# Optimization experiments

Measured on AMD Instinct MI355X. Metric: run time of the kernel, lower is better.

Reference implementation:

```python
import jax, jax.numpy as jnp
import numpy as np

N = 30000   # nodes
E = 240000  # edges
G = 16      # graphs in batch
DIMS = [1, 256, 512, 1024]
OUT = 1024

def _xavier(key, fan_in, fan_out):
    lim = float(np.sqrt(6.0 / (fan_in + fan_out)))
    return jax.random.uniform(key, (fan_in, fan_out), minval=-lim, maxval=lim, dtype=jnp.float32)

def setup_inputs() -> dict:
    key = jax.random.key(0)
    ks = jax.random.split(key, 8)
    x = jax.random.normal(ks[0], (N, DIMS[0]), dtype=jnp.float32)
    edge_index = jax.random.randint(ks[1], (2, E), 0, N, dtype=jnp.int64)
    batch = jnp.sort(jax.random.randint(ks[2], (N,), 0, G, dtype=jnp.int64))
    W1 = _xavier(ks[3], DIMS[0], DIMS[1]); b1 = jnp.zeros((DIMS[1],), jnp.float32)
    W2 = _xavier(ks[4], DIMS[1], DIMS[2]); b2 = jnp.zeros((DIMS[2],), jnp.float32)
    W3 = _xavier(ks[5], DIMS[2], DIMS[3]); b3 = jnp.zeros((DIMS[3],), jnp.float32)
    Wo = _xavier(ks[6], DIMS[3], OUT);     bo = jnp.zeros((OUT,), jnp.float32)
    return {"x": x, "edge_index": edge_index, "batch": batch,
            "W1": W1, "b1": b1, "W2": W2, "b2": b2, "W3": W3, "b3": b3,
            "Wo": Wo, "bo": bo}

def reference(x, edge_index, batch, W1, b1, W2, b2, W3, b3, Wo, bo):
    n = x.shape[0]
    loops = jnp.arange(n)
    # GCNConv adds self-loops, then symmetric deg^-1/2 normalization
    src = jnp.concatenate([edge_index[0], loops])
    dst = jnp.concatenate([edge_index[1], loops])
    deg = jnp.zeros((n,), jnp.float32).at[dst].add(1.0)  # >=1 due to self-loops
    dis = jax.lax.rsqrt(deg)
    norm = (dis[src] * dis[dst])[:, None]  # [E+N, 1]

    def gcn(h, W, b):
        h = h @ W                                   # linear (no bias in lin)
        agg = jnp.zeros_like(h).at[dst].add(h[src] * norm)  # scatter-add messages
        return agg + b                              # GCNConv bias

    h = jax.nn.relu(gcn(x, W1, b1))
    h = jax.nn.relu(gcn(h, W2, b2))
    h = jax.nn.relu(gcn(h, W3, b3))
    # global mean pool over graphs
    sums = jnp.zeros((G, h.shape[1]), h.dtype).at[batch].add(h)
    cnt = jnp.zeros((G,), h.dtype).at[batch].add(1.0)
    pooled = sums / jnp.maximum(cnt, 1.0)[:, None]
    return pooled @ Wo + bo
```

## Files before the change

kernel.cpp:

```cpp
#include <hip/hip_runtime.h>
#include <hip/hip_bf16.h>
#include <stdint.h>

#define N_NODES 30000
#define E_EDGES 240000
#define NGRAPH  16
#define D1      256
#define D2      512
#define D3      1024
#define DOUT    1024
#define M_PAD   30720
#define NT_M    240
#define CAP     40

typedef unsigned short ushort_t;
typedef short short8 __attribute__((ext_vector_type(8)));
typedef float f32x4 __attribute__((ext_vector_type(4)));

__device__ __forceinline__ float bf2f(ushort_t u) {
    union { unsigned int i; float f; } v; v.i = ((unsigned int)u) << 16; return v.f;
}
__device__ __forceinline__ ushort_t f2bf(float x) {
    union { float f; unsigned int i; } v; v.f = x;
    unsigned int r = v.i + 0x7fffu + ((v.i >> 16) & 1u);
    return (ushort_t)(r >> 16);
}

__device__ __forceinline__ void gl_lds16(const ushort_t* g, ushort_t* l) {
    __builtin_amdgcn_global_load_lds(
        (const __attribute__((address_space(1))) void*)(g),
        (__attribute__((address_space(3))) void*)(l), 16, 0, 0);
}

__global__ void k_detect(const void* w1, const void* ei, int* flags) {
    int lane = threadIdx.x & 63;
    const ushort_t* h = (const ushort_t*)w1;
    float v = fabsf(bf2f(h[lane * 2]));
    unsigned long long badf = __ballot(!(v <= 0.25f));
    const int* e = (const int*)ei;
    unsigned long long badi = __ballot(e[lane * 2 + 1] != 0);
    if (threadIdx.x == 0) {
        flags[0] = (badf == 0ull) ? 1 : 0;
        flags[1] = (badi == 0ull) ? 1 : 0;
    }
}

__global__ void k_setup(const void* x, const void* batch, const void* w1, const void* b1,
                        const void* b2, const void* b3, const void* bo,
                        const void* W2, const void* W3,
                        float* xf, int* batch32, float* W1f, float* b1f, float* b2f,
                        float* b3f, float* bof, ushort_t* Wt2, ushort_t* Wt3,
                        int* slotcnt, float* pooled, float* pooled2, const int* flags) {
    int isbf = flags[0];
    int bid = blockIdx.x;
    int tid = threadIdx.x;
    if (bid < 492) {
        int i = bid * 256 + tid;
        if (i < 3072) {
            const void* src; float* dst; int idx;
            if      (i < 256)  { src = w1; dst = W1f; idx = i; }
            else if (i < 512)  { src = b1; dst = b1f; idx = i - 256; }
            else if (i < 1024) { src = b2; dst = b2f; idx = i - 512; }
            else if (i < 2048) { src = b3; dst = b3f; idx = i - 1024; }
            else               { src = bo; dst = bof; idx = i - 2048; }
            dst[idx] = isbf ? bf2f(((const ushort_t*)src)[idx]) : ((const float*)src)[idx];
        } else if (i < 33072) {
            int idx = i - 3072;
            xf[idx] = isbf ? bf2f(((const ushort_t*)x)[idx]) : ((const float*)x)[idx];
        } else if (i < 63072) {
            int idx = i - 33072;
            batch32[idx] = flags[1] ? (int)((const long long*)batch)[idx]
                                    : ((const int*)batch)[idx];
        } else if (i < 93072) {
            slotcnt[i - 63072] = 0;
        } else if (i < 109456) {
            pooled[i - 93072] = 0.0f;
        } else if (i < 125840) {
            pooled2[i - 109456] = 0.0f;
        }
    } else {
        __shared__ ushort_t tile[32][33];
        int tb = bid - 492;
        const void* in; ushort_t* out; int R, C, bx, by;
        if (tb < 128) { in = W2; out = Wt2; R = D1; C = D2; bx = tb & 15; by = tb >> 4; }
        else { tb -= 128; in = W3; out = Wt3; R = D2; C = D3; bx = tb & 31; by = tb >> 5; }
        int tx = tid & 31, ty = tid >> 5;
        int c0 = bx * 32, r0 = by * 32;
        for (int i = ty; i < 32; i += 8) {
            size_t idx = (size_t)(r0 + i) * C + c0 + tx;
            tile[i][tx] = isbf ? ((const ushort_t*)in)[idx] : f2bf(((const float*)in)[idx]);
        }
        __syncthreads();
        for (int i = ty; i < 32; i += 8) out[(size_t)(c0 + i) * R + r0 + tx] = tile[tx][i];
    }
}

__global__ void k_edge_count(const void* ei, int* slotcnt, int* slots, const int* flags) {
    int e = blockIdx.x * 256 + threadIdx.x;
    if (e >= E_EDGES) return;
    int s, d;
    if (flags[1]) {
        s = (int)((const long long*)ei)[e];
        d = (int)((const long long*)ei)[E_EDGES + e];
    } else {
        s = ((const int*)ei)[e];
        d = ((const int*)ei)[E_EDGES + e];
    }
    if ((unsigned)s >= N_NODES || (unsigned)d >= N_NODES) return;
    int pos = atomicAdd(&slotcnt[d], 1);
    if (pos < CAP) slots[d * CAP + pos] = s;
}

__global__ void k_s1(const float* xf, const int* slotcnt, const int* slots,
                     const int* batch, float* dis, float* s1, float* cntg) {
    int b = blockIdx.x;
    if (b == 118) {
        int g = threadIdx.x;
        if (g >= NGRAPH) return;
        int lo0 = 0, hi0 = N_NODES;
        while (lo0 < hi0) { int m = (lo0 + hi0) >> 1; if (batch[m] < g) lo0 = m + 1; else hi0 = m; }
        int lo1 = lo0, hi1 = N_NODES;
        while (lo1 < hi1) { int m = (lo1 + hi1) >> 1; if (batch[m] < g + 1) lo1 = m + 1; else hi1 = m; }
        cntg[g] = (float)(lo1 - lo0);
        return;
    }
    int d = b * 256 + threadIdx.x;
    if (d >= N_NODES) return;
    int cd = slotcnt[d];
    float di = rsqrtf(1.0f + (float)cd);
    dis[d] = di;
    int cnt = cd < CAP ? cd : CAP;
    float acc = xf[d] * di;
    for (int k = 0; k < cnt; k++) {
        int s = slots[d * CAP + k];
        acc += xf[s] * rsqrtf(1.0f + (float)slotcnt[s]);
    }
    s1[d] = acc * di;
}

__global__ void k_agg1(const float* s1, const float* W1f, const float* b1f,
                       ushort_t* a2, const int* slots, const int* slotcnt, const float* dis) {
    int node = blockIdx.x * 4 + (threadIdx.x >> 6);
    int lane = threadIdx.x & 63;
    int c4 = lane * 4;
    float w[4], bb[4], a[4];
    #pragma unroll
    for (int j = 0; j < 4; j++) { w[j] = W1f[c4 + j]; bb[j] = b1f[c4 + j]; }
    float di = dis[node];
    int cnt = slotcnt[node]; cnt = cnt < CAP ? cnt : CAP;
    float sv = s1[node];
    float wsl = di * di;
    #pragma unroll
    for (int j = 0; j < 4; j++) a[j] = wsl * fmaxf(sv * w[j] + bb[j], 0.0f);
    for (int k = 0; k < cnt; k++) {
        int s = slots[node * CAP + k];
        float ss = s1[s];
        float wn = dis[s] * di;
        #pragma unroll
        for (int j = 0; j < 4; j++) a[j] += wn * fmaxf(ss * w[j] + bb[j], 0.0f);
    }
    uint2 o;
    o.x = (unsigned int)f2bf(a[0]) | ((unsigned int)f2bf(a[1]) << 16);
    o.y = (unsigned int)f2bf(a[2]) | ((unsigned int)f2bf(a[3]) << 16);
    *(uint2*)&a2[(size_t)node * D1 + c4] = o;
}

__global__ void k_agg2(const ushort_t* h, ushort_t* out, const int* slots,
                       const int* slotcnt, const float* dis) {
    int node = blockIdx.x * 4 + (threadIdx.x >> 6);
    int lane = threadIdx.x & 63;
    int c8 = lane * 8;
    float di = dis[node];
    int cnt = slotcnt[node]; cnt = cnt < CAP ? cnt : CAP;
    float w = di * di;
    const ushort_t* hp = h + c8;
    short8 p = *(const short8*)&hp[(size_t)node * D2];
    float a[8];
    #pragma unroll
    for (int j = 0; j < 8; j++) a[j] = w * bf2f((ushort_t)p[j]);
    if (cnt > 0) {
        int s0 = slots[node * CAP];
        short8 q0 = *(const short8*)&hp[(size_t)s0 * D2];
        float ws0 = dis[s0] * di;
        for (int k = 1; k < cnt; k++) {
            int s1i = slots[node * CAP + k];
            short8 q1 = *(const short8*)&hp[(size_t)s1i * D2];
            float ws1 = dis[s1i] * di;
            #pragma unroll
            for (int j = 0; j < 8; j++) a[j] += ws0 * bf2f((ushort_t)q0[j]);
            q0 = q1; ws0 = ws1;
        }
        #pragma unroll
        for (int j = 0; j < 8; j++) a[j] += ws0 * bf2f((ushort_t)q0[j]);
    }
    uint4 o;
    o.x = (unsigned int)f2bf(a[0]) | ((unsigned int)f2bf(a[1]) << 16);
    o.y = (unsigned int)f2bf(a[2]) | ((unsigned int)f2bf(a[3]) << 16);
    o.z = (unsigned int)f2bf(a[4]) | ((unsigned int)f2bf(a[5]) << 16);
    o.w = (unsigned int)f2bf(a[6]) | ((unsigned int)f2bf(a[7]) << 16);
    *(uint4*)&out[(size_t)node * D2 + c8] = o;
}

__global__ __launch_bounds__(256, 3) void k_gemm(const ushort_t* A, const ushort_t* Bt,
                                                 const float* bias, ushort_t* Cmat,
                                                 int K, int Ncols, int ntn) {
    __shared__ __align__(16) ushort_t As[2][128 * 32];
    __shared__ __align__(16) ushort_t Bs[2][128 * 32];
    int tid = threadIdx.x;
    int id = blockIdx.x;
    int xcd = id & 7, q = id >> 3;
    int rt = xcd * (NT_M / 8) + q / ntn;
    int ct = q % ntn;
    int bm0 = rt * 128, bn0 = ct * 128;
    int wave = tid >> 6, lane = tid & 63;
    int wm = (wave & 1) * 64, wn = (wave >> 1) * 64;
    int l15 = lane & 15, quad = lane >> 4;

    int m1 = tid >> 2, k1 = (tid & 3) << 3;
    int m2 = m1 + 64;
    int off1 = m1 * 32 + k1, off2 = m2 * 32 + k1;
    const ushort_t* pA1 = A + (size_t)(bm0 + m1) * K + k1;
    const ushort_t* pA2 = A + (size_t)(bm0 + m2) * K + k1;
    const ushort_t* pB1 = Bt + (size_t)(bn0 + m1) * K + k1;
    const ushort_t* pB2 = Bt + (size_t)(bn0 + m2) * K + k1;

    {
        uint4 la0 = *(const uint4*)pA1, la1 = *(const uint4*)pA2;
        uint4 lb0 = *(const uint4*)pB1, lb1 = *(const uint4*)pB2;
        *(uint4*)&As[0][off1] = la0; *(uint4*)&As[0][off2] = la1;
        *(uint4*)&Bs[0][off1] = lb0; *(uint4*)&Bs[0][off2] = lb1;
    }

    f32x4 acc[4][4];
    for (int a = 0; a < 4; a++)
        for (int b = 0; b < 4; b++)
            acc[a][b] = (f32x4){0.f, 0.f, 0.f, 0.f};

    int niter = K >> 5;
    for (int it = 0; it < niter; ++it) {
        __syncthreads();
        int ktn = (it + 1) << 5;
        uint4 na0, na1, nb0, nb1;
        if (ktn < K) {
            na0 = *(const uint4*)(pA1 + ktn); na1 = *(const uint4*)(pA2 + ktn);
            nb0 = *(const uint4*)(pB1 + ktn); nb1 = *(const uint4*)(pB2 + ktn);
        }
        int cb = it & 1;
        short8 af[4], bfr[4];
        for (int im = 0; im < 4; im++)
            af[im] = *(const short8*)&As[cb][(wm + im * 16 + l15) * 32 + quad * 8];
        for (int in = 0; in < 4; in++)
            bfr[in] = *(const short8*)&Bs[cb][(wn + in * 16 + l15) * 32 + quad * 8];
        for (int im = 0; im < 4; im++)
            for (int in = 0; in < 4; in++)
                acc[im][in] = __builtin_amdgcn_mfma_f32_16x16x32_bf16(af[im], bfr[in], acc[im][in], 0, 0, 0);
        if (ktn < K) {
            int wb = cb ^ 1;
            *(uint4*)&As[wb][off1] = na0; *(uint4*)&As[wb][off2] = na1;
            *(uint4*)&Bs[wb][off1] = nb0; *(uint4*)&Bs[wb][off2] = nb1;
        }
    }

    for (int im = 0; im < 4; im++) {
        int row = bm0 + wm + im * 16 + quad * 4;
        for (int in = 0; in < 4; in++) {
            int col = bn0 + wn + in * 16 + l15;
            float bv = bias[col];
            for (int r = 0; r < 4; r++) {
                float v = acc[im][in][r] + bv;
                v = v > 0.0f ? v : 0.0f;
                Cmat[(size_t)(row + r) * Ncols + col] = f2bf(v);
            }
        }
    }
}

#define GPHASE(M0, M1, PRESTAGE, TAILWAIT)                                             \
    a0 = rdA(slot, M0, inrow0); a1 = rdA(slot, M0, inrow1);                            \
    a2r = rdA(slot, M1, inrow0); a3r = rdA(slot, M1, inrow1);                          \
    PRESTAGE                                                                           \
    asm volatile("" ::: "memory");                                                     \
    __builtin_amdgcn_s_barrier();                                                      \
    asm volatile("s_waitcnt lgkmcnt(0)" ::: "memory");                                 \
    __builtin_amdgcn_sched_barrier(0);                                                 \
    __builtin_amdgcn_s_setprio(1);                                                     \
    _Pragma("unroll")                                                                  \
    for (int n = 0; n < 4; ++n) {                                                      \
        acc[M0][n] = __builtin_amdgcn_mfma_f32_16x16x32_bf16(a0,  bf_[n][0], acc[M0][n], 0, 0, 0); \
        acc[M0][n] = __builtin_amdgcn_mfma_f32_16x16x32_bf16(a1,  bf_[n][1], acc[M0][n], 0, 0, 0); \
        acc[M1][n] = __builtin_amdgcn_mfma_f32_16x16x32_bf16(a2r, bf_[n][0], acc[M1][n], 0, 0, 0); \
        acc[M1][n] = __builtin_amdgcn_mfma_f32_16x16x32_bf16(a3r, bf_[n][1], acc[M1][n], 0, 0, 0); \
    }                                                                                  \
    __builtin_amdgcn_s_setprio(0);                                                     \
    TAILWAIT                                                                           \
    asm volatile("" ::: "memory");                                                     \
    __builtin_amdgcn_s_barrier();

#define PS_ALL  if (hn) { stage_unit(nslot, t + 1, 0); stage_unit(nslot, t + 1, 1);    \
                          stage_unit(nslot, t + 1, 2); stage_unit(nslot, t + 1, 3); }
#define PS_NONE
#define TW_NONE
#define TW_P2 if (hn) { asm volatile("s_waitcnt vmcnt(8)" ::: "memory"); } \
              else    { asm volatile("s_waitcnt vmcnt(0)" ::: "memory"); }
#define TW_P4 if (hn) { asm volatile("s_waitcnt vmcnt(2)" ::: "memory"); }

__global__ __launch_bounds__(512, 2) void k_gemm8p(const ushort_t* A, const ushort_t* Bt,
                                                   const float* bias, const int* batch,
                                                   float* pooled, int K, int ntn, int NT) {
    __shared__ __align__(16) ushort_t As[2][256 * 64];
    __shared__ __align__(16) ushort_t Bs[2][256 * 64];
    const int tid = threadIdx.x;
    const int id = blockIdx.x;
    const int xcd = id & 7, q = id >> 3;
    const int rt = xcd * ((M_PAD / 256) / 8) + q / ntn;
    const int ct = q % ntn;
    const int bm0 = rt * 256, bn0 = ct * 256;
    const int wave = tid >> 6, lane = tid & 63;
    const int wr = wave >> 2, wc = wave & 3;
    const int l15 = lane & 15, quad = lane >> 4;

    const ushort_t* gA = A + (size_t)bm0 * K;
    const ushort_t* gB = Bt + (size_t)bn0 * K;

    auto stage_blk = [&](ushort_t* ldsbase, const ushort_t* gbase, int kt, int b) {
        int row = b >> 3;
        int kb = (b & 7) ^ (row & 7);
        gl_lds16(gbase + (size_t)row * K + (kt << 6) + (kb << 3), ldsbase + (b << 3));
    };
    auto stage_unit = [&](int slot, int kt, int u) {
        if (u == 0)      { stage_blk(Bs[slot], gB, kt, tid);        stage_blk(Bs[slot], gB, kt, tid + 512); }
        else if (u == 1) { stage_blk(Bs[slot], gB, kt, tid + 1024); stage_blk(Bs[slot], gB, kt, tid + 1536); }
        else if (u == 2) { stage_blk(As[slot], gA, kt, tid);        stage_blk(As[slot], gA, kt, tid + 1024); }
        else             { stage_blk(As[slot], gA, kt, tid + 512);  stage_blk(As[slot], gA, kt, tid + 1536); }
    };

    const int swzx = (l15 & 7) << 4;
    const int inrow0 = (quad * 16) ^ swzx;
    const int inrow1 = (quad * 16 + 64) ^ swzx;
    const int arowb = (wr * 128 + l15) * 128;
    const int browb = (wc * 64 + l15) * 128;

    auto rdA = [&](int slot, int m, int inr) -> short8 {
        return *(const short8*)((const char*)As[slot] + arowb + m * 2048 + inr);
    };
    auto rdB = [&](int slot, int n, int inr) -> short8 {
        return *(const short8*)((const char*)Bs[slot] + browb + n * 2048 + inr);
    };

    stage_unit(0, 0, 0); stage_unit(0, 0, 1); stage_unit(0, 0, 2); stage_unit(0, 0, 3);
    asm volatile("s_waitcnt vmcnt(2)" ::: "memory");
    __builtin_amdgcn_s_barrier();

    f32x4 acc[8][4];
    #pragma unroll
    for (int a = 0; a < 8; a++)
        #pragma unroll
        for (int b = 0; b < 4; b++)
            acc[a][b] = (f32x4){0.f, 0.f, 0.f, 0.f};

    short8 bf_[4][2];
    for (int t = 0; t < NT; ++t) {
        const int slot = t & 1, nslot = slot ^ 1;
        const bool hn = (t + 1) < NT;
        short8 a0, a1, a2r, a3r;
        #pragma unroll
        for (int n = 0; n < 4; ++n) {
            bf_[n][0] = rdB(slot, n, inrow0);
            bf_[n][1] = rdB(slot, n, inrow1);
        }
        GPHASE(0, 1, PS_ALL, TW_NONE)
        GPHASE(2, 3, PS_NONE, TW_P2)
        GPHASE(4, 5, PS_NONE, TW_NONE)
        GPHASE(6, 7, PS_NONE, TW_P4)
    }

    asm volatile("s_waitcnt vmcnt(0) lgkmcnt(0)" ::: "memory");
    __syncthreads();
    float* pl = (float*)&As[0][0];
    int* gtile = (int*)&Bs[0][0];
    for (int i = tid; i < NGRAPH * 256; i += 512) pl[i] = 0.0f;
    if (tid < 256) {
        int r = bm0 + tid; if (r > N_NODES - 1) r = N_NODES - 1;
        int g = batch[r]; g = g < 0 ? 0 : (g > NGRAPH - 1 ? NGRAPH - 1 : g);
        gtile[tid] = g;
    }
    __syncthreads();

    int gmin = gtile[0], gmax = gtile[255];
    if (gmin == gmax && bm0 + 255 < N_NODES) {
        float csum[4];
        float bv[4];
        #pragma unroll
        for (int in = 0; in < 4; in++) {
            csum[in] = 0.0f;
            bv[in] = bias[bn0 + wc * 64 + in * 16 + l15];
        }
        #pragma unroll
        for (int im = 0; im < 8; im++) {
            #pragma unroll
            for (int in = 0; in < 4; in++) {
                #pragma unroll
                for (int r = 0; r < 4; r++)
                    csum[in] += fmaxf(acc[im][in][r] + bv[in], 0.0f);
            }
        }
        #pragma unroll
        for (int in = 0; in < 4; in++) {
            csum[in] += __shfl_xor(csum[in], 16);
            csum[in] += __shfl_xor(csum[in], 32);
        }
        if (quad == 0) {
            #pragma unroll
            for (int in = 0; in < 4; in++)
                atomicAdd(&pl[gmin * 256 + wc * 64 + in * 16 + l15], csum[in]);
        }
    } else {
        #pragma unroll
        for (int im = 0; im < 8; im++) {
            int rl = wr * 128 + im * 16 + quad * 4;
            #pragma unroll
            for (int in = 0; in < 4; in++) {
                int cl = wc * 64 + in * 16 + l15;
                float bv = bias[bn0 + cl];
                float vsum = 0.0f;
                int gprev = gtile[rl];
                #pragma unroll
                for (int r = 0; r < 4; r++) {
                    int row = bm0 + rl + r;
                    float v = (row < N_NODES) ? fmaxf(acc[im][in][r] + bv, 0.0f) : 0.0f;
                    int g = gtile[rl + r];
                    if (g != gprev) {
                        atomicAdd(&pl[gprev * 256 + cl], vsum);
                        vsum = 0.0f; gprev = g;
                    }
                    vsum += v;
                }
                atomicAdd(&pl[gprev * 256 + cl], vsum);
            }
        }
    }
    __syncthreads();

    int span = (gmax - gmin + 1) * 256;
    for (int idx = tid; idx < span; idx += 512) {
        int g = gmin + (idx >> 8), cl = idx & 255;
        float v = pl[g * 256 + cl];
        if (v != 0.0f) atomicAdd(&pooled[g * DOUT + bn0 + cl], v);
    }
}

__global__ __launch_bounds__(256) void k_out_partial(const float* pooled, const void* Wo,
                                                     float* pooled2, const int* flags) {
    __shared__ float pl[NGRAPH * 32];
    int tid = threadIdx.x;
    int col = blockIdx.x * 256 + tid;
    int k0 = blockIdx.y * 32;
    for (int i = tid; i < NGRAPH * 32; i += 256) {
        int g = i >> 5, kk = i & 31;
        pl[i] = pooled[g * D3 + k0 + kk];
    }
    __syncthreads();
    int isbf = flags[0];
    float acc[NGRAPH];
    #pragma unroll
    for (int g = 0; g < NGRAPH; g++) acc[g] = 0.0f;
    #pragma unroll 4
    for (int kk = 0; kk < 32; kk++) {
        int k = k0 + kk;
        float wv = isbf ? bf2f(((const ushort_t*)Wo)[(size_t)k * DOUT + col])
                        : ((const float*)Wo)[(size_t)k * DOUT + col];
        #pragma unroll
        for (int g = 0; g < NGRAPH; g++)
            acc[g] += pl[g * 32 + kk] * wv;
    }
    #pragma unroll
    for (int g = 0; g < NGRAPH; g++)
        atomicAdd(&pooled2[g * DOUT + col], acc[g]);
}

__global__ void k_out_fin(const float* pooled2, const float* bof, const float* cntg,
                          void* out, const int* flags) {
    int i = blockIdx.x * 256 + threadIdx.x;
    int g = i >> 10, o = i & 1023;
    float c = cntg[g]; c = c > 1.0f ? c : 1.0f;
    float v = pooled2[i] / c + bof[o];
    if (flags[0]) ((ushort_t*)out)[i] = f2bf(v);
    else          ((float*)out)[i] = v;
}

extern "C" void kernel_launch(void* const* d_in, const int* in_sizes, int n_in,
                              void* d_out, int out_size, void* d_ws, size_t ws_size,
                              hipStream_t stream) {
    const void* x_raw  = d_in[0];
    const void* ei_raw = d_in[1];
    const void* b_raw  = d_in[2];
    const void* W1_raw = d_in[3];
    const void* b1_raw = d_in[4];
    const void* W2_raw = d_in[5];
    const void* b2_raw = d_in[6];
    const void* W3_raw = d_in[7];
    const void* b3_raw = d_in[8];
    const void* Wo_raw = d_in[9];
    const void* bo_raw = d_in[10];

    char* w = (char*)d_ws;
    size_t off = 0;
    auto alloc = [&](size_t b) { size_t o = off; off += (b + 255) & ~(size_t)255; return o; };
    int*   flags   = (int*)  (w + alloc(256));
    float* xf      = (float*)(w + alloc((size_t)N_NODES * 4));
    int*   batch32 = (int*)  (w + alloc((size_t)N_NODES * 4));
    float* W1f     = (float*)(w + alloc(D1 * 4));
    float* b1f     = (float*)(w + alloc(D1 * 4));
    float* b2f     = (float*)(w + alloc(D2 * 4));
    float* b3f     = (float*)(w + alloc(D3 * 4));
    float* bof     = (float*)(w + alloc(DOUT * 4));
    float* dis     = (float*)(w + alloc((size_t)N_NODES * 4));
    float* s1      = (float*)(w + alloc((size_t)N_NODES * 4));
    float* cntg    = (float*)(w + alloc(64));
    float* pooled  = (float*)(w + alloc((size_t)NGRAPH * DOUT * 4));
    float* pooled2 = (float*)(w + alloc((size_t)NGRAPH * DOUT * 4));
    int*   slotcnt = (int*)  (w + alloc((size_t)N_NODES * 4));
    int*   slots   = (int*)  (w + alloc((size_t)N_NODES * CAP * 4));
    ushort_t* Wt2  = (ushort_t*)(w + alloc((size_t)D2 * D1 * 2));
    ushort_t* Wt3  = (ushort_t*)(w + alloc((size_t)D3 * D2 * 2));
    ushort_t* slabA = (ushort_t*)(w + alloc((size_t)M_PAD * D2 * 2));
    ushort_t* a2 = slabA;
    ushort_t* a3 = slabA;
    ushort_t* h2   = (ushort_t*)(w + alloc((size_t)M_PAD * D2 * 2));

    int nb_e = (E_EDGES + 255) / 256;

    k_detect<<<1, 64, 0, stream>>>(W1_raw, ei_raw, flags);
    k_setup<<<1132, 256, 0, stream>>>(x_raw, b_raw, W1_raw, b1_raw, b2_raw, b3_raw, bo_raw,
                                      W2_raw, W3_raw, xf, batch32, W1f, b1f, b2f, b3f, bof,
                                      Wt2, Wt3, slotcnt, pooled, pooled2, flags);
    k_edge_count<<<nb_e, 256, 0, stream>>>(ei_raw, slotcnt, slots, flags);
    k_s1<<<119, 256, 0, stream>>>(xf, slotcnt, slots, batch32, dis, s1, cntg);

    k_agg1<<<N_NODES / 4, 256, 0, stream>>>(s1, W1f, b1f, a2, slots, slotcnt, dis);
    k_gemm<<<NT_M * (D2 / 128), 256, 0, stream>>>(a2, Wt2, b2f, h2, D1, D2, D2 / 128);
    k_agg2<<<N_NODES / 4, 256, 0, stream>>>(h2, a3, slots, slotcnt, dis);
    k_gemm8p<<<(M_PAD / 256) * (D3 / 256), 512, 0, stream>>>(a3, Wt3, b3f, batch32,
                                                             pooled, D2, D3 / 256, D2 / 64);

    k_out_partial<<<dim3(DOUT / 256, D3 / 32), 256, 0, stream>>>(pooled, Wo_raw, pooled2, flags);
    k_out_fin<<<NGRAPH * DOUT / 256, 256, 0, stream>>>(pooled2, bof, cntg, d_out, flags);
}
```

Before: 272.3 us.

## Broadcast neighbor indices via shuffles and simplify fused GEMM pipeline

In the two aggregation kernels, each lane now loads one neighbor slot index and its normalization weight up front, and the neighbor loop pulls these with wave shuffles. This replaces the serial per-iteration loads of slot, dis and s1. Separately, the fused layer-3 GEMM+pool kernel drops its hand-scheduled phase macros (split staging, explicit vmcnt waits, setprio, sched barriers) in favor of a plain double-buffered loop: stage the next tile, run the MFMAs, then __syncthreads. This simplifies the code but risks losing the fine-grained overlap of global-to-LDS loads with MFMA work.

New measurement: 254.8 us. 1.07x faster.

```diff
diff --git a/kernel.cpp b/kernel.cpp
--- a/kernel.cpp
+++ b/kernel.cpp
@@ -148,14 +148,16 @@
     for (int j = 0; j < 4; j++) { w[j] = W1f[c4 + j]; bb[j] = b1f[c4 + j]; }
     float di = dis[node];
     int cnt = slotcnt[node]; cnt = cnt < CAP ? cnt : CAP;
+    int s_l = (lane < cnt) ? slots[node * CAP + lane] : 0;
+    float wn_l = dis[s_l] * di;
+    float ss_l = s1[s_l];
     float sv = s1[node];
     float wsl = di * di;
     #pragma unroll
     for (int j = 0; j < 4; j++) a[j] = wsl * fmaxf(sv * w[j] + bb[j], 0.0f);
     for (int k = 0; k < cnt; k++) {
-        int s = slots[node * CAP + k];
-        float ss = s1[s];
-        float wn = dis[s] * di;
+        float ss = __shfl(ss_l, k);
+        float wn = __shfl(wn_l, k);
         #pragma unroll
         for (int j = 0; j < 4; j++) a[j] += wn * fmaxf(ss * w[j] + bb[j], 0.0f);
     }
@@ -172,6 +174,8 @@
     int c8 = lane * 8;
     float di = dis[node];
     int cnt = slotcnt[node]; cnt = cnt < CAP ? cnt : CAP;
+    int s_l = (lane < cnt) ? slots[node * CAP + lane] : 0;
+    float ws_l = dis[s_l] * di;
     float w = di * di;
     const ushort_t* hp = h + c8;
     short8 p = *(const short8*)&hp[(size_t)node * D2];
@@ -179,13 +183,13 @@
     #pragma unroll
     for (int j = 0; j < 8; j++) a[j] = w * bf2f((ushort_t)p[j]);
     if (cnt > 0) {
-        int s0 = slots[node * CAP];
+        int s0 = __shfl(s_l, 0);
+        float ws0 = __shfl(ws_l, 0);
         short8 q0 = *(const short8*)&hp[(size_t)s0 * D2];
-        float ws0 = dis[s0] * di;
         for (int k = 1; k < cnt; k++) {
-            int s1i = slots[node * CAP + k];
-            short8 q1 = *(const short8*)&hp[(size_t)s1i * D2];
-            float ws1 = dis[s1i] * di;
+            int sk = __shfl(s_l, k);
+            float ws1 = __shfl(ws_l, k);
+            short8 q1 = *(const short8*)&hp[(size_t)sk * D2];
             #pragma unroll
             for (int j = 0; j < 8; j++) a[j] += ws0 * bf2f((ushort_t)q0[j]);
             q0 = q1; ws0 = ws1;
@@ -275,38 +279,9 @@
     }
 }
 
-#define GPHASE(M0, M1, PRESTAGE, TAILWAIT)                                             \
-    a0 = rdA(slot, M0, inrow0); a1 = rdA(slot, M0, inrow1);                            \
-    a2r = rdA(slot, M1, inrow0); a3r = rdA(slot, M1, inrow1);                          \
-    PRESTAGE                                                                           \
-    asm volatile("" ::: "memory");                                                     \
-    __builtin_amdgcn_s_barrier();                                                      \
-    asm volatile("s_waitcnt lgkmcnt(0)" ::: "memory");                                 \
-    __builtin_amdgcn_sched_barrier(0);                                                 \
-    __builtin_amdgcn_s_setprio(1);                                                     \
-    _Pragma("unroll")                                                                  \
-    for (int n = 0; n < 4; ++n) {                                                      \
-        acc[M0][n] = __builtin_amdgcn_mfma_f32_16x16x32_bf16(a0,  bf_[n][0], acc[M0][n], 0, 0, 0); \
-        acc[M0][n] = __builtin_amdgcn_mfma_f32_16x16x32_bf16(a1,  bf_[n][1], acc[M0][n], 0, 0, 0); \
-        acc[M1][n] = __builtin_amdgcn_mfma_f32_16x16x32_bf16(a2r, bf_[n][0], acc[M1][n], 0, 0, 0); \
-        acc[M1][n] = __builtin_amdgcn_mfma_f32_16x16x32_bf16(a3r, bf_[n][1], acc[M1][n], 0, 0, 0); \
-    }                                                                                  \
-    __builtin_amdgcn_s_setprio(0);                                                     \
-    TAILWAIT                                                                           \
-    asm volatile("" ::: "memory");                                                     \
-    __builtin_amdgcn_s_barrier();
-
-#define PS_ALL  if (hn) { stage_unit(nslot, t + 1, 0); stage_unit(nslot, t + 1, 1);    \
-                          stage_unit(nslot, t + 1, 2); stage_unit(nslot, t + 1, 3); }
-#define PS_NONE
-#define TW_NONE
-#define TW_P2 if (hn) { asm volatile("s_waitcnt vmcnt(8)" ::: "memory"); } \
-              else    { asm volatile("s_waitcnt vmcnt(0)" ::: "memory"); }
-#define TW_P4 if (hn) { asm volatile("s_waitcnt vmcnt(2)" ::: "memory"); }
-
-__global__ __launch_bounds__(512, 2) void k_gemm8p(const ushort_t* A, const ushort_t* Bt,
-                                                   const float* bias, const int* batch,
-                                                   float* pooled, int K, int ntn, int NT) {
+__global__ __launch_bounds__(512, 2) void k_gemm_pool(const ushort_t* A, const ushort_t* Bt,
+                                                      const float* bias, const int* batch,
+                                                      float* pooled, int K, int ntn, int NT) {
     __shared__ __align__(16) ushort_t As[2][256 * 64];
     __shared__ __align__(16) ushort_t Bs[2][256 * 64];
     const int tid = threadIdx.x;
@@ -327,11 +302,11 @@
         int kb = (b & 7) ^ (row & 7);
         gl_lds16(gbase + (size_t)row * K + (kt << 6) + (kb << 3), ldsbase + (b << 3));
     };
-    auto stage_unit = [&](int slot, int kt, int u) {
-        if (u == 0)      { stage_blk(Bs[slot], gB, kt, tid);        stage_blk(Bs[slot], gB, kt, tid + 512); }
-        else if (u == 1) { stage_blk(Bs[slot], gB, kt, tid + 1024); stage_blk(Bs[slot], gB, kt, tid + 1536); }
-        else if (u == 2) { stage_blk(As[slot], gA, kt, tid);        stage_blk(As[slot], gA, kt, tid + 1024); }
-        else             { stage_blk(As[slot], gA, kt, tid + 512);  stage_blk(As[slot], gA, kt, tid + 1536); }
+    auto stage_all = [&](int slot, int kt) {
+        stage_blk(Bs[slot], gB, kt, tid);        stage_blk(Bs[slot], gB, kt, tid + 512);
+        stage_blk(Bs[slot], gB, kt, tid + 1024); stage_blk(Bs[slot], gB, kt, tid + 1536);
+        stage_blk(As[slot], gA, kt, tid);        stage_blk(As[slot], gA, kt, tid + 512);
+        stage_blk(As[slot], gA, kt, tid + 1024); stage_blk(As[slot], gA, kt, tid + 1536);
     };
 
     const int swzx = (l15 & 7) << 4;
@@ -347,9 +322,8 @@
         return *(const short8*)((const char*)Bs[slot] + browb + n * 2048 + inr);
     };
 
-    stage_unit(0, 0, 0); stage_unit(0, 0, 1); stage_unit(0, 0, 2); stage_unit(0, 0, 3);
-    asm volatile("s_waitcnt vmcnt(2)" ::: "memory");
-    __builtin_amdgcn_s_barrier();
+    stage_all(0, 0);
+    __syncthreads();
 
     f32x4 acc[8][4];
     #pragma unroll
@@ -358,24 +332,30 @@
         for (int b = 0; b < 4; b++)
             acc[a][b] = (f32x4){0.f, 0.f, 0.f, 0.f};
 
-    short8 bf_[4][2];
     for (int t = 0; t < NT; ++t) {
-        const int slot = t & 1, nslot = slot ^ 1;
-        const bool hn = (t + 1) < NT;
-        short8 a0, a1, a2r, a3r;
+        const int slot = t & 1;
+        if (t + 1 < NT) stage_all(slot ^ 1, t + 1);
+        short8 bf_[4][2];
         #pragma unroll
         for (int n = 0; n < 4; ++n) {
             bf_[n][0] = rdB(slot, n, inrow0);
             bf_[n][1] = rdB(slot, n, inrow1);
         }
-        GPHASE(0, 1, PS_ALL, TW_NONE)
-        GPHASE(2, 3, PS_NONE, TW_P2)
-        GPHASE(4, 5, PS_NONE, TW_NONE)
-        GPHASE(6, 7, PS_NONE, TW_P4)
-    }
-
-    asm volatile("s_waitcnt vmcnt(0) lgkmcnt(0)" ::: "memory");
-    __syncthreads();
+        #pragma unroll
+        for (int mp = 0; mp < 4; ++mp) {
+            short8 a0 = rdA(slot, 2 * mp, inrow0), a1 = rdA(slot, 2 * mp, inrow1);
+            short8 a2r = rdA(slot, 2 * mp + 1, inrow0), a3r = rdA(slot, 2 * mp + 1, inrow1);
+            #pragma unroll
+            for (int n = 0; n < 4; ++n) {
+                acc[2 * mp][n]     = __builtin_amdgcn_mfma_f32_16x16x32_bf16(a0,  bf_[n][0], acc[2 * mp][n], 0, 0, 0);
+                acc[2 * mp][n]     = __builtin_amdgcn_mfma_f32_16x16x32_bf16(a1,  bf_[n][1], acc[2 * mp][n], 0, 0, 0);
+                acc[2 * mp + 1][n] = __builtin_amdgcn_mfma_f32_16x16x32_bf16(a2r, bf_[n][0], acc[2 * mp + 1][n], 0, 0, 0);
+                acc[2 * mp + 1][n] = __builtin_amdgcn_mfma_f32_16x16x32_bf16(a3r, bf_[n][1], acc[2 * mp + 1][n], 0, 0, 0);
+            }
+        }
+        __syncthreads();
+    }
+
     float* pl = (float*)&As[0][0];
     int* gtile = (int*)&Bs[0][0];
     for (int i = tid; i < NGRAPH * 256; i += 512) pl[i] = 0.0f;
@@ -540,8 +520,8 @@
     k_agg1<<<N_NODES / 4, 256, 0, stream>>>(s1, W1f, b1f, a2, slots, slotcnt, dis);
     k_gemm<<<NT_M * (D2 / 128), 256, 0, stream>>>(a2, Wt2, b2f, h2, D1, D2, D2 / 128);
     k_agg2<<<N_NODES / 4, 256, 0, stream>>>(h2, a3, slots, slotcnt, dis);
-    k_gemm8p<<<(M_PAD / 256) * (D3 / 256), 512, 0, stream>>>(a3, Wt3, b3f, batch32,
-                                                             pooled, D2, D3 / 256, D2 / 64);
+    k_gemm_pool<<<(M_PAD / 256) * (D3 / 256), 512, 0, stream>>>(a3, Wt3, b3f, batch32,
+                                                                pooled, D2, D3 / 256, D2 / 64);
 
     k_out_partial<<<dim3(DOUT / 256, D3 / 32), 256, 0, stream>>>(pooled, Wo_raw, pooled2, flags);
     k_out_fin<<<NGRAPH * DOUT / 256, 256, 0, stream>>>(pooled2, bof, cntg, d_out, flags);
```
